# Performance work log

Hardware: AMD Instinct MI355X
Metric: run time of the kernel (lower is better)

Reference implementation:

```python
import jax, jax.numpy as jnp
import numpy as np

INT_MIN = jnp.iinfo(jnp.int32).min


def setup_inputs() -> dict:
    key = jax.random.key(0)
    ks = jax.random.split(key, 12)
    N, E, H, R, T = 200000, 100000, 100, 172, 100
    return {
        'src': jax.random.randint(ks[0], (E,), 0, N, dtype=jnp.int32),
        'dst': jax.random.randint(ks[1], (E,), 0, N, dtype=jnp.int32),
        't': jax.random.randint(ks[2], (E,), 0, 1000000, dtype=jnp.int32),
        'raw_msg': jax.random.normal(ks[3], (E, R), dtype=jnp.float32),
        'memory': jax.random.normal(ks[4], (N, H), dtype=jnp.float32),
        'last_update': jax.random.randint(ks[5], (N,), 0, 1000, dtype=jnp.int32),
        'te_w': jax.random.normal(ks[6], (T, 1), dtype=jnp.float32) * 0.1,
        'te_b': jax.random.normal(ks[7], (T,), dtype=jnp.float32) * 0.1,
        'w_ih': jax.random.normal(ks[8], (3 * H, 2 * H + R + T), dtype=jnp.float32) * 0.05,
        'w_hh': jax.random.normal(ks[9], (3 * H, H), dtype=jnp.float32) * 0.05,
        'b_ih': jax.random.normal(ks[10], (3 * H,), dtype=jnp.float32) * 0.05,
        'b_hh': jax.random.normal(ks[11], (3 * H,), dtype=jnp.float32) * 0.05,
    }


def reference(src, dst, t, raw_msg, memory, last_update, te_w, te_b, w_ih, w_hh, b_ih, b_hh):
    N, H = memory.shape
    E = src.shape[0]

    def time_enc(t_rel):  # Linear(1, time_dim) then cos, t_rel: [E] float
        return jnp.cos(t_rel[:, None] * te_w[:, 0][None, :] + te_b[None, :])

    # IdentityMessage: concat(mem[src], mem[dst], raw_msg, t_enc); two streams (s and d)
    t_enc_s = time_enc((t - last_update[src]).astype(raw_msg.dtype))
    t_enc_d = time_enc((t - last_update[dst]).astype(raw_msg.dtype))
    msg_s = jnp.concatenate([memory[src], memory[dst], raw_msg, t_enc_s], axis=-1)
    msg_d = jnp.concatenate([memory[dst], memory[src], raw_msg, t_enc_d], axis=-1)

    msg = jnp.concatenate([msg_s, msg_d], axis=0)        # [2E, msg_dim]
    idx = jnp.concatenate([src, dst], axis=0)            # [2E]
    t2 = jnp.concatenate([t, t], axis=0)                 # [2E]

    # LastAggregator: per node pick the message with maximum timestamp
    max_t = jnp.full((N,), INT_MIN, dtype=t2.dtype).at[idx].max(t2)
    cand = jnp.where(t2 == max_t[idx], jnp.arange(2 * E, dtype=jnp.int32), jnp.int32(-1))
    win = jnp.full((N,), -1, dtype=jnp.int32).at[idx].max(cand)  # winning edge per node
    has_msg = win >= 0
    aggr = jnp.where(has_msg[:, None], msg[jnp.clip(win, 0)], 0.0)  # [N, msg_dim]

    # GRUCell(msg_dim, H)
    gi = aggr @ w_ih.T + b_ih                             # [N, 3H]
    gh = memory @ w_hh.T + b_hh                           # [N, 3H]
    i_r, i_z, i_n = jnp.split(gi, 3, axis=-1)
    h_r, h_z, h_n = jnp.split(gh, 3, axis=-1)
    r = jax.nn.sigmoid(i_r + h_r)
    z = jax.nn.sigmoid(i_z + h_z)
    n = jnp.tanh(i_n + r * h_n)
    memory_new = (1.0 - z) * n + z * memory               # [N, H]

    last_update_new = last_update.at[idx].max(t2)         # scatter latest event time
    return memory_new, last_update_new
```

## Files before the change

kernel.cpp:

```cpp
#include <hip/hip_runtime.h>
#include <math.h>

typedef __attribute__((ext_vector_type(8))) short  short8;
typedef __attribute__((ext_vector_type(4))) float  f32x4;

static constexpr int H     = 100;
static constexpr int RD    = 172;
static constexpr int WK    = 472;
static constexpr int MSTR  = 104;
static constexpr int RSTR  = 176;
static constexpr int NKS   = 20;
static constexpr int MB    = 32;
static constexpr int GRPS  = 2;
static constexpr int BLK   = 448;
static constexpr int NTT   = 28;
static constexpr int BPK_N = NTT * NKS * 64 * 8;

static constexpr int FB_MB = 48;
static constexpr int FB_GR = 3;

__device__ inline unsigned short f2bf(float x) {
    union { float f; unsigned u; } v; v.f = x;
    return (unsigned short)((v.u + 0x7FFFu + ((v.u >> 16) & 1u)) >> 16);
}
__device__ inline float bf2f(unsigned short b) {
    union { unsigned u; float f; } v; v.u = ((unsigned)b) << 16;
    return v.f;
}
__device__ inline unsigned pkbf(float a, float b) {
    unsigned r;
    asm("v_cvt_pk_bf16_f32 %0, %1, %2" : "=v"(r) : "v"(a), "v"(b));
    return r;
}
__device__ inline float frcp(float x) {
    float r;
    asm("v_rcp_f32 %0, %1" : "=v"(r) : "v"(x));
    return r;
}
__device__ inline f32x4 mfma16(short8 a, short8 b, f32x4 c) {
    return __builtin_amdgcn_mfma_f32_16x16x32_bf16(a, b, c, 0, 0, 0);
}
__device__ inline float4 ld4g(const float* base, int lc, int limit) {
    if (lc + 4 <= limit) return *(const float4*)(base + lc);
    return make_float4(0.f, 0.f, 0.f, 0.f);
}
__device__ inline void gl16(const unsigned short* g, unsigned short* l) {
    __builtin_amdgcn_global_load_lds(
        (const __attribute__((address_space(1))) void*)g,
        (__attribute__((address_space(3))) void*)l, 16, 0, 0);
}

__global__ __launch_bounds__(256) void k_init(int* __restrict__ maxt, int* __restrict__ win,
                                              int* __restrict__ zb, int N) {
    int i = blockIdx.x * blockDim.x + threadIdx.x;
    if (i < N) { maxt[i] = (int)0x80000000; win[i] = -1; }
    if (i < 128) zb[i] = 0;
}
__global__ __launch_bounds__(256) void k_maxt(const int* __restrict__ src, const int* __restrict__ dst,
                                              const int* __restrict__ t, int* __restrict__ maxt, int E) {
    int j = blockIdx.x * blockDim.x + threadIdx.x;
    if (j < E) {
        int tj = t[j];
        atomicMax(&maxt[src[j]], tj);
        atomicMax(&maxt[dst[j]], tj);
    }
}
__global__ __launch_bounds__(256) void k_win(const int* __restrict__ src, const int* __restrict__ dst,
                                             const int* __restrict__ t, const int* __restrict__ maxt,
                                             int* __restrict__ win, int E) {
    int j = blockIdx.x * blockDim.x + threadIdx.x;
    if (j < E) {
        int tj = t[j];
        int s = src[j], d = dst[j];
        if (maxt[s] == tj) atomicMax(&win[s], j);
        if (maxt[d] == tj) atomicMax(&win[d], j + E);
    }
}
__global__ __launch_bounds__(256) void k_meta(const int* __restrict__ src, const int* __restrict__ dst,
                                              const int* __restrict__ t, const int* __restrict__ last_update,
                                              const int* __restrict__ win, int4* __restrict__ meta,
                                              float* __restrict__ out_lu, int E, int N) {
    int i = blockIdx.x * blockDim.x + threadIdx.x;
    if (i >= N) return;
    int lu = last_update[i], w = win[i];
    int j = 0, other = 0, has = 0, te = lu; float dt = 0.f;
    if (w >= 0) {
        has = 1;
        int e = (w < E) ? w : (w - E);
        j = e;
        other = (w < E) ? dst[e] : src[e];
        te = t[e];
        dt = (float)(te - lu);
    }
    out_lu[i] = (float)(te > lu ? te : lu);
    int4 m; m.x = j; m.y = other; m.z = has; m.w = __float_as_int(dt);
    meta[i] = m;
}

__global__ __launch_bounds__(256) void k_cvt(const float* __restrict__ mem, const float* __restrict__ raw,
                                             unsigned short* __restrict__ memB, unsigned short* __restrict__ rawB,
                                             int N, int E) {
    int i = blockIdx.x * 256 + threadIdx.x;
    const int nm = N * 13;
    if (i < nm) {
        int row = i / 13, o = (i - row * 13) * 8;
        float4 a = ld4g(mem + (size_t)row * 100, o, 100);
        float4 b = ld4g(mem + (size_t)row * 100, o + 4, 100);
        int4 s; s.x = (int)pkbf(a.x, a.y); s.y = (int)pkbf(a.z, a.w);
        s.z = (int)pkbf(b.x, b.y); s.w = (int)pkbf(b.z, b.w);
        *(int4*)&memB[(size_t)row * MSTR + o] = s;
    } else if (i < nm + E * 22) {
        int k = i - nm;
        int row = k / 22, o = (k - row * 22) * 8;
        float4 a = ld4g(raw + (size_t)row * 172, o, 172);
        float4 b = ld4g(raw + (size_t)row * 172, o + 4, 172);
        int4 s; s.x = (int)pkbf(a.x, a.y); s.y = (int)pkbf(a.z, a.w);
        s.z = (int)pkbf(b.x, b.y); s.w = (int)pkbf(b.z, b.w);
        *(int4*)&rawB[(size_t)row * RSTR + o] = s;
    }
}

__global__ __launch_bounds__(256) void k_prep(const float* __restrict__ w_ih, const float* __restrict__ w_hh,
                                              unsigned short* __restrict__ B) {
    int idx = blockIdx.x * 256 + threadIdx.x;
    if (idx >= BPK_N) return;
    int jj   = idx & 7;
    int lane = (idx >> 3) & 63;
    int rest = idx >> 9;
    int ks   = rest % NKS;
    int tile = rest / NKS;
    int kk   = ks * 32 + ((lane >> 4) << 3) + jj;
    float v = 0.f;
    if (tile < 21) {
        int gate = tile / 7;
        int tcol = (tile % 7) * 16 + (lane & 15);
        if (tcol < 100) {
            if (kk < 512) {
                int col = -1;
                if (kk < 100)                   col = kk;
                else if (kk >= 104 && kk < 204) col = kk - 4;
                else if (kk >= 208 && kk < 380) col = kk - 8;
                else if (kk >= 384 && kk < 484) col = kk - 12;
                if (col >= 0) v = w_ih[(gate * 100 + tcol) * WK + col];
            } else {
                int khh = kk - 512;
                if (gate < 2 && khh < 100)
                    v = w_hh[(gate * 100 + tcol) * H + khh];
            }
        }
    } else {
        int tcol = (tile - 21) * 16 + (lane & 15);
        int khh  = kk - 512;
        if (tcol < 100 && khh >= 0 && khh < 100)
            v = w_hh[(200 + tcol) * H + khh];
    }
    B[idx] = f2bf(v);
}

__global__ __launch_bounds__(BLK, 7) void k_gru2(
    const unsigned short* __restrict__ memB, const unsigned short* __restrict__ rawB,
    const float* __restrict__ te_w, const float* __restrict__ te_b,
    const float* __restrict__ b_ih, const float* __restrict__ b_hh,
    const int4* __restrict__ meta, const unsigned short* __restrict__ zb,
    const unsigned short* __restrict__ Bpack,
    float* __restrict__ out_mem, int N)
{
    __shared__ unsigned short sA[GRPS * NKS * 512];

    const int tid  = threadIdx.x;
    const int wv   = tid >> 6;
    const int lane = tid & 63;
    const int q    = lane >> 4;
    const int row  = lane & 15;
    const int node0 = blockIdx.x * MB;

#pragma unroll
    for (int g = 0; g < GRPS; ++g) {
        const int node_g = node0 + g * 16 + row;
        const bool val = node_g < N;
        const int4 m = val ? meta[node_g] : make_int4(0, 0, 0, 0);
        const bool has = m.z != 0;
        const float dt = __int_as_float(m.w);
        const unsigned short* pmm = has ? memB + (size_t)node_g * MSTR : zb;
        const unsigned short* pot = has ? memB + (size_t)m.y * MSTR   : zb;
        const unsigned short* prw = has ? rawB + (size_t)m.x * RSTR   : zb;
        const unsigned short* phh = val ? memB + (size_t)node_g * MSTR : zb;

#pragma unroll
        for (int ii = 0; ii < 3; ++ii) {
            const int ks = wv + 7 * ii;
            if (ks < NKS && (ks < 12 || ks >= 16)) {
                const int k0 = ks * 32 + q * 8;
                const unsigned short* s =
                    (k0 < 104) ? pmm + k0 :
                    (k0 < 208) ? pot + (k0 - 104) :
                    (k0 < 384) ? prw + (k0 - 208) :
                                 phh + (k0 - 512);
                gl16(s, &sA[(g * NKS + ks) * 512]);
            }
        }
#pragma unroll
        for (int ii = 0; ii < 3; ++ii) {
            const int ks = wv + 7 * ii;
            if (ks >= 12 && ks < 16) {
                const int o = (ks - 12) * 32 + q * 8;
                float4 w0 = ld4g(te_w, o, 100), w1 = ld4g(te_w, o + 4, 100);
                float4 c0 = ld4g(te_b, o, 100), c1 = ld4g(te_b, o + 4, 100);
                const float hf = has ? 1.f : 0.f;
                float v0 = hf * __cosf(fmaf(dt, w0.x, c0.x));
                float v1 = hf * __cosf(fmaf(dt, w0.y, c0.y));
                float v2 = hf * __cosf(fmaf(dt, w0.z, c0.z));
                float v3 = hf * __cosf(fmaf(dt, w0.w, c0.w));
                float v4 = hf * __cosf(fmaf(dt, w1.x, c1.x));
                float v5 = hf * __cosf(fmaf(dt, w1.y, c1.y));
                float v6 = hf * __cosf(fmaf(dt, w1.z, c1.z));
                float v7 = hf * __cosf(fmaf(dt, w1.w, c1.w));
                int4 sv;
                sv.x = (int)pkbf(v0, v1); sv.y = (int)pkbf(v2, v3);
                sv.z = (int)pkbf(v4, v5); sv.w = (int)pkbf(v6, v7);
                *(int4*)&sA[(g * NKS + ks) * 512 + lane * 8] = sv;
            }
        }
    }
    __syncthreads();

    f32x4 ar[GRPS], az[GRPS], an[GRPS], ah[GRPS];
#pragma unroll
    for (int m = 0; m < GRPS; ++m) { ar[m] = (f32x4)0.f; az[m] = (f32x4)0.f; an[m] = (f32x4)0.f; ah[m] = (f32x4)0.f; }

    __builtin_amdgcn_s_setprio(1);
#pragma unroll
    for (int ks = 0; ks < NKS; ++ks) {
        short8 a0 = *(const short8*)&sA[(0 * NKS + ks) * 512 + lane * 8];
        short8 a1 = *(const short8*)&sA[(1 * NKS + ks) * 512 + lane * 8];
        short8 br = *(const short8*)&Bpack[(((size_t)(     wv) * NKS + ks) * 64 + lane) * 8];
        short8 bz = *(const short8*)&Bpack[(((size_t)( 7 + wv) * NKS + ks) * 64 + lane) * 8];
        short8 bn = (ks < 16)
                  ? *(const short8*)&Bpack[(((size_t)(14 + wv) * NKS + ks) * 64 + lane) * 8]
                  : *(const short8*)&Bpack[(((size_t)(21 + wv) * NKS + ks) * 64 + lane) * 8];
        ar[0] = mfma16(a0, br, ar[0]);  ar[1] = mfma16(a1, br, ar[1]);
        az[0] = mfma16(a0, bz, az[0]);  az[1] = mfma16(a1, bz, az[1]);
        if (ks < 16) { an[0] = mfma16(a0, bn, an[0]);  an[1] = mfma16(a1, bn, an[1]); }
        else         { ah[0] = mfma16(a0, bn, ah[0]);  ah[1] = mfma16(a1, bn, ah[1]); }
    }
    __builtin_amdgcn_s_setprio(0);

    const int c = wv * 16 + row;
    if (c < 100) {
        const float br_ = b_ih[c]       + b_hh[c];
        const float bz_ = b_ih[c + 100] + b_hh[c + 100];
        const float bin = b_ih[c + 200];
        const float bhn = b_hh[c + 200];
        const int ksh = 16 + (c >> 5);
        const int qh  = (c >> 3) & 3;
        const int e   = c & 7;
#pragma unroll
        for (int m = 0; m < GRPS; ++m) {
#pragma unroll
            for (int r = 0; r < 4; ++r) {
                const int node = node0 + m * 16 + q * 4 + r;
                if (node < N) {
                    const int rw = q * 4 + r;
                    const float h  = bf2f(sA[(m * NKS + ksh) * 512 + (qh * 16 + rw) * 8 + e]);
                    const float rg = frcp(1.f + __expf(-(ar[m][r] + br_)));
                    const float zg = frcp(1.f + __expf(-(az[m][r] + bz_)));
                    const float xn = an[m][r] + bin + rg * (ah[m][r] + bhn);
                    const float th = copysignf(1.f - 2.f * frcp(__expf(2.f * fabsf(xn)) + 1.f), xn);
                    out_mem[(size_t)node * H + c] = (1.f - zg) * th + zg * h;
                }
            }
        }
    }
}

__global__ __launch_bounds__(BLK, 4) void k_gru_fused(
    const int* __restrict__ src, const int* __restrict__ dst, const int* __restrict__ t,
    const float* __restrict__ raw_msg, const float* __restrict__ memory,
    const int* __restrict__ last_update, const float* __restrict__ te_w,
    const float* __restrict__ te_b, const float* __restrict__ b_ih,
    const float* __restrict__ b_hh, const int* __restrict__ win,
    const unsigned short* __restrict__ Bpack,
    float* __restrict__ out_mem, float* __restrict__ out_lu, int E, int N)
{
    __shared__ unsigned short sA[FB_GR * NKS * 512];
    __shared__ int   s_other[FB_MB];
    __shared__ int   s_j[FB_MB];
    __shared__ int   s_has[FB_MB];
    __shared__ float s_dt[FB_MB];

    const int tid   = threadIdx.x;
    const int node0 = blockIdx.x * FB_MB;

    if (tid < FB_MB) {
        int node = node0 + tid;
        int has = 0, j = 0, other = 0; float dt = 0.f;
        if (node < N) {
            int lu = last_update[node];
            int w  = win[node];
            int te = lu;
            if (w >= 0) {
                has = 1;
                int e = (w < E) ? w : (w - E);
                j = e;
                other = (w < E) ? dst[e] : src[e];
                te = t[e];
                dt = (float)(te - lu);
            }
            out_lu[node] = (float)(te > lu ? te : lu);
        }
        s_j[tid] = j; s_other[tid] = other; s_has[tid] = has; s_dt[tid] = dt;
    }
    __syncthreads();

    if (tid < 432) {
        const int nl    = tid % 48;
        const int c0    = tid / 48;
        const int node  = node0 + nl;
        const bool valid = node < N;
        const int has   = s_has[nl];
        const float* memN = memory + (size_t)node * H;
        const float* memO = memory + (size_t)s_other[nl] * H;
        const float* rawJ = raw_msg + (size_t)s_j[nl] * RD;
        const float dt  = s_dt[nl];
        const int grp = nl >> 4;
        const int row = nl & 15;

        float4 va[8], vb[8];
#pragma unroll
        for (int it = 0; it < 8; ++it) {
            const int cc = c0 + it * 9;
            va[it] = make_float4(0.f, 0.f, 0.f, 0.f); vb[it] = va[it];
            if (cc < 67) {
                const int c = cc + 13, kb = c * 8;
                if (c < 26)      { if (has)  { va[it] = ld4g(memO, kb - 104, 100); vb[it] = ld4g(memO, kb - 100, 100); } }
                else if (c < 48) { if (has)  { va[it] = ld4g(rawJ, kb - 208, RD ); vb[it] = ld4g(rawJ, kb - 204, RD ); } }
                else if (c < 64) { }
                else             { if (valid){ va[it] = ld4g(memN, kb - 512, 100); vb[it] = ld4g(memN, kb - 508, 100); } }
            }
        }
#pragma unroll
        for (int it = 0; it < 8; ++it) {
            const int cc = c0 + it * 9;
            if (cc < 67) {
                const int c = cc + 13;
                if (c >= 48 && c < 64 && has) {
                    const int lc = c * 8 - 384;
                    float vv[8];
#pragma unroll
                    for (int x = 0; x < 8; ++x) {
                        int col = lc + x;
                        vv[x] = (col < 100) ? __cosf(fmaf(dt, te_w[col], te_b[col])) : 0.f;
                    }
                    va[it] = make_float4(vv[0], vv[1], vv[2], vv[3]);
                    vb[it] = make_float4(vv[4], vv[5], vv[6], vv[7]);
                }
                int4 sv;
                sv.x = (int)pkbf(va[it].x, va[it].y);
                sv.y = (int)pkbf(va[it].z, va[it].w);
                sv.z = (int)pkbf(vb[it].x, vb[it].y);
                sv.w = (int)pkbf(vb[it].z, vb[it].w);
                {
                    const int ks = c >> 2, sub = c & 3;
                    *(int4*)&sA[((grp * NKS + ks) * 64 + sub * 16 + row) * 8] = sv;
                }
                if (c >= 64 && c < 77) {
                    int4 sm_;
                    sm_.x = has ? sv.x : 0; sm_.y = has ? sv.y : 0;
                    sm_.z = has ? sv.z : 0; sm_.w = has ? sv.w : 0;
                    const int cm = c - 64;
                    const int ks = cm >> 2, sub = cm & 3;
                    *(int4*)&sA[((grp * NKS + ks) * 64 + sub * 16 + row) * 8] = sm_;
                }
            }
        }
    }
    __syncthreads();

    const int wv   = tid >> 6;
    const int lane = tid & 63;
    const int lrow = lane & 15;
    const int lhi  = lane >> 4;

    f32x4 ar[FB_GR], az[FB_GR], an[FB_GR], ah[FB_GR];
#pragma unroll
    for (int m = 0; m < FB_GR; ++m) { ar[m] = (f32x4)0.f; az[m] = (f32x4)0.f; an[m] = (f32x4)0.f; ah[m] = (f32x4)0.f; }

    __builtin_amdgcn_s_setprio(1);
#pragma unroll
    for (int ks = 0; ks < NKS; ++ks) {
        short8 a0 = *(const short8*)&sA[(0 * NKS + ks) * 512 + lane * 8];
        short8 a1 = *(const short8*)&sA[(1 * NKS + ks) * 512 + lane * 8];
        short8 a2 = *(const short8*)&sA[(2 * NKS + ks) * 512 + lane * 8];
        short8 br = *(const short8*)&Bpack[(((size_t)(     wv) * NKS + ks) * 64 + lane) * 8];
        short8 bz = *(const short8*)&Bpack[(((size_t)( 7 + wv) * NKS + ks) * 64 + lane) * 8];
        short8 bn = (ks < 16)
                  ? *(const short8*)&Bpack[(((size_t)(14 + wv) * NKS + ks) * 64 + lane) * 8]
                  : *(const short8*)&Bpack[(((size_t)(21 + wv) * NKS + ks) * 64 + lane) * 8];
        ar[0] = mfma16(a0, br, ar[0]);  ar[1] = mfma16(a1, br, ar[1]);  ar[2] = mfma16(a2, br, ar[2]);
        az[0] = mfma16(a0, bz, az[0]);  az[1] = mfma16(a1, bz, az[1]);  az[2] = mfma16(a2, bz, az[2]);
        if (ks < 16) { an[0] = mfma16(a0, bn, an[0]);  an[1] = mfma16(a1, bn, an[1]);  an[2] = mfma16(a2, bn, an[2]); }
        else         { ah[0] = mfma16(a0, bn, ah[0]);  ah[1] = mfma16(a1, bn, ah[1]);  ah[2] = mfma16(a2, bn, ah[2]); }
    }
    __builtin_amdgcn_s_setprio(0);

    const int c = wv * 16 + lrow;
    if (c < 100) {
        const float br_ = b_ih[c]       + b_hh[c];
        const float bz_ = b_ih[c + 100] + b_hh[c + 100];
        const float bin = b_ih[c + 200];
        const float bhn = b_hh[c + 200];
        const int ksh = 16 + (c >> 5);
        const int qh  = (c >> 3) & 3;
        const int e   = c & 7;
#pragma unroll
        for (int m = 0; m < FB_GR; ++m) {
#pragma unroll
            for (int r = 0; r < 4; ++r) {
                const int node = node0 + m * 16 + lhi * 4 + r;
                if (node < N) {
                    const int rw = lhi * 4 + r;
                    const float h  = bf2f(sA[(m * NKS + ksh) * 512 + (qh * 16 + rw) * 8 + e]);
                    const float rg = frcp(1.f + __expf(-(ar[m][r] + br_)));
                    const float zg = frcp(1.f + __expf(-(az[m][r] + bz_)));
                    const float xn = an[m][r] + bin + rg * (ah[m][r] + bhn);
                    const float th = copysignf(1.f - 2.f * frcp(__expf(2.f * fabsf(xn)) + 1.f), xn);
                    out_mem[(size_t)node * H + c] = (1.f - zg) * th + zg * h;
                }
            }
        }
    }
}

extern "C" void kernel_launch(void* const* d_in, const int* in_sizes, int n_in,
                              void* d_out, int out_size, void* d_ws, size_t ws_size,
                              hipStream_t stream)
{
    const int*   src         = (const int*)d_in[0];
    const int*   dst         = (const int*)d_in[1];
    const int*   t           = (const int*)d_in[2];
    const float* raw_msg     = (const float*)d_in[3];
    const float* memory      = (const float*)d_in[4];
    const int*   last_update = (const int*)d_in[5];
    const float* te_w        = (const float*)d_in[6];
    const float* te_b        = (const float*)d_in[7];
    const float* w_ih        = (const float*)d_in[8];
    const float* w_hh        = (const float*)d_in[9];
    const float* b_ih        = (const float*)d_in[10];
    const float* b_hh        = (const float*)d_in[11];

    const int E = in_sizes[0];
    const int N = in_sizes[5];

    float* out    = (float*)d_out;
    float* out_lu = out + (size_t)N * H;

    char* ws = (char*)d_ws;
    int* maxt = (int*)ws;
    int* win  = maxt + N;
    unsigned short* Bpack = (unsigned short*)(win + N);
    int4* meta = (int4*)(Bpack + BPK_N);
    unsigned short* zb   = (unsigned short*)(meta + N);
    unsigned short* memB = zb + 256;
    unsigned short* rawB = memB + (size_t)N * MSTR + 32;
    const size_t need = (size_t)((char*)(rawB + (size_t)E * RSTR) - ws) + 64;

    k_init<<<(N + 255) / 256, 256, 0, stream>>>(maxt, win, (int*)zb, N);
    k_prep<<<(BPK_N + 255) / 256, 256, 0, stream>>>(w_ih, w_hh, Bpack);
    k_maxt<<<(E + 255) / 256, 256, 0, stream>>>(src, dst, t, maxt, E);
    k_win <<<(E + 255) / 256, 256, 0, stream>>>(src, dst, t, maxt, win, E);

    if (ws_size >= need) {
        const int ncvt = N * 13 + E * 22;
        k_cvt<<<(ncvt + 255) / 256, 256, 0, stream>>>(memory, raw_msg, memB, rawB, N, E);
        k_meta<<<(N + 255) / 256, 256, 0, stream>>>(src, dst, t, last_update, win, meta, out_lu, E, N);
        k_gru2<<<(N + MB - 1) / MB, BLK, 0, stream>>>(memB, rawB, te_w, te_b, b_ih, b_hh,
                                                      meta, zb, Bpack, out, N);
    } else {
        k_gru_fused<<<(N + FB_MB - 1) / FB_MB, BLK, 0, stream>>>(src, dst, t, raw_msg, memory, last_update,
                                                                 te_w, te_b, b_ih, b_hh, win, Bpack,
                                                                 out, out_lu, E, N);
    }
}
```

Baseline: 205.8 us.

## Merge init/prep/convert kernels and software-pipeline B-tile loads in GRU MFMA loop

Merges k_init, k_prep and k_cvt into one k_pre launch, which removes two kernel launches and their serialization gaps. Inside k_gru2 the per-k-step global loads of the weight fragments are now double-buffered: the next step's B fragments are fetched before the current step's MFMAs, with a sched_barrier to stop the compiler reordering them. The launch-bounds occupancy hint drops from 7 to 4 waves to allow more registers for the prefetch buffers. The cost is lower occupancy and more register pressure.

```diff
diff --git a/kernel.cpp b/kernel.cpp
--- a/kernel.cpp
+++ b/kernel.cpp
@@ -50,12 +50,78 @@
         (__attribute__((address_space(3))) void*)l, 16, 0, 0);
 }
 
-__global__ __launch_bounds__(256) void k_init(int* __restrict__ maxt, int* __restrict__ win,
-                                              int* __restrict__ zb, int N) {
-    int i = blockIdx.x * blockDim.x + threadIdx.x;
+__global__ __launch_bounds__(256) void k_pre(
+    const float* __restrict__ mem, const float* __restrict__ raw,
+    const float* __restrict__ w_ih, const float* __restrict__ w_hh,
+    unsigned short* __restrict__ memB, unsigned short* __restrict__ rawB,
+    unsigned short* __restrict__ B, int* __restrict__ maxt, int* __restrict__ win,
+    int* __restrict__ zb, int N, int E, int docvt)
+{
+    int i = blockIdx.x * 256 + threadIdx.x;
+    if (docvt) {
+        const int nm = N * 13;
+        if (i < nm) {
+            int row = i / 13, o = (i - row * 13) * 8;
+            float4 a = ld4g(mem + (size_t)row * 100, o, 100);
+            float4 b = ld4g(mem + (size_t)row * 100, o + 4, 100);
+            int4 s; s.x = (int)pkbf(a.x, a.y); s.y = (int)pkbf(a.z, a.w);
+            s.z = (int)pkbf(b.x, b.y); s.w = (int)pkbf(b.z, b.w);
+            *(int4*)&memB[(size_t)row * MSTR + o] = s;
+            return;
+        }
+        i -= nm;
+        const int nr = E * 22;
+        if (i < nr) {
+            int row = i / 22, o = (i - row * 22) * 8;
+            float4 a = ld4g(raw + (size_t)row * 172, o, 172);
+            float4 b = ld4g(raw + (size_t)row * 172, o + 4, 172);
+            int4 s; s.x = (int)pkbf(a.x, a.y); s.y = (int)pkbf(a.z, a.w);
+            s.z = (int)pkbf(b.x, b.y); s.w = (int)pkbf(b.z, b.w);
+            *(int4*)&rawB[(size_t)row * RSTR + o] = s;
+            return;
+        }
+        i -= nr;
+    }
+    if (i < BPK_N) {
+        int idx  = i;
+        int jj   = idx & 7;
+        int lane = (idx >> 3) & 63;
+        int rest = idx >> 9;
+        int ks   = rest % NKS;
+        int tile = rest / NKS;
+        int kk   = ks * 32 + ((lane >> 4) << 3) + jj;
+        float v = 0.f;
+        if (tile < 21) {
+            int gate = tile / 7;
+            int tcol = (tile % 7) * 16 + (lane & 15);
+            if (tcol < 100) {
+                if (kk < 512) {
+                    int col = -1;
+                    if (kk < 100)                   col = kk;
+                    else if (kk >= 104 && kk < 204) col = kk - 4;
+                    else if (kk >= 208 && kk < 380) col = kk - 8;
+                    else if (kk >= 384 && kk < 484) col = kk - 12;
+                    if (col >= 0) v = w_ih[(gate * 100 + tcol) * WK + col];
+                } else {
+                    int khh = kk - 512;
+                    if (gate < 2 && khh < 100)
+                        v = w_hh[(gate * 100 + tcol) * H + khh];
+                }
+            }
+        } else {
+            int tcol = (tile - 21) * 16 + (lane & 15);
+            int khh  = kk - 512;
+            if (tcol < 100 && khh >= 0 && khh < 100)
+                v = w_hh[(200 + tcol) * H + khh];
+        }
+        B[idx] = f2bf(v);
+        return;
+    }
+    i -= BPK_N;
     if (i < N) { maxt[i] = (int)0x80000000; win[i] = -1; }
     if (i < 128) zb[i] = 0;
 }
+
 __global__ __launch_bounds__(256) void k_maxt(const int* __restrict__ src, const int* __restrict__ dst,
                                               const int* __restrict__ t, int* __restrict__ maxt, int E) {
     int j = blockIdx.x * blockDim.x + threadIdx.x;
@@ -97,67 +163,9 @@
     meta[i] = m;
 }
 
-__global__ __launch_bounds__(256) void k_cvt(const float* __restrict__ mem, const float* __restrict__ raw,
-                                             unsigned short* __restrict__ memB, unsigned short* __restrict__ rawB,
-                                             int N, int E) {
-    int i = blockIdx.x * 256 + threadIdx.x;
-    const int nm = N * 13;
-    if (i < nm) {
-        int row = i / 13, o = (i - row * 13) * 8;
-        float4 a = ld4g(mem + (size_t)row * 100, o, 100);
-        float4 b = ld4g(mem + (size_t)row * 100, o + 4, 100);
-        int4 s; s.x = (int)pkbf(a.x, a.y); s.y = (int)pkbf(a.z, a.w);
-        s.z = (int)pkbf(b.x, b.y); s.w = (int)pkbf(b.z, b.w);
-        *(int4*)&memB[(size_t)row * MSTR + o] = s;
-    } else if (i < nm + E * 22) {
-        int k = i - nm;
-        int row = k / 22, o = (k - row * 22) * 8;
-        float4 a = ld4g(raw + (size_t)row * 172, o, 172);
-        float4 b = ld4g(raw + (size_t)row * 172, o + 4, 172);
-        int4 s; s.x = (int)pkbf(a.x, a.y); s.y = (int)pkbf(a.z, a.w);
-        s.z = (int)pkbf(b.x, b.y); s.w = (int)pkbf(b.z, b.w);
-        *(int4*)&rawB[(size_t)row * RSTR + o] = s;
-    }
-}
-
-__global__ __launch_bounds__(256) void k_prep(const float* __restrict__ w_ih, const float* __restrict__ w_hh,
-                                              unsigned short* __restrict__ B) {
-    int idx = blockIdx.x * 256 + threadIdx.x;
-    if (idx >= BPK_N) return;
-    int jj   = idx & 7;
-    int lane = (idx >> 3) & 63;
-    int rest = idx >> 9;
-    int ks   = rest % NKS;
-    int tile = rest / NKS;
-    int kk   = ks * 32 + ((lane >> 4) << 3) + jj;
-    float v = 0.f;
-    if (tile < 21) {
-        int gate = tile / 7;
-        int tcol = (tile % 7) * 16 + (lane & 15);
-        if (tcol < 100) {
-            if (kk < 512) {
-                int col = -1;
-                if (kk < 100)                   col = kk;
-                else if (kk >= 104 && kk < 204) col = kk - 4;
-                else if (kk >= 208 && kk < 380) col = kk - 8;
-                else if (kk >= 384 && kk < 484) col = kk - 12;
-                if (col >= 0) v = w_ih[(gate * 100 + tcol) * WK + col];
-            } else {
-                int khh = kk - 512;
-                if (gate < 2 && khh < 100)
-                    v = w_hh[(gate * 100 + tcol) * H + khh];
-            }
-        }
-    } else {
-        int tcol = (tile - 21) * 16 + (lane & 15);
-        int khh  = kk - 512;
-        if (tcol < 100 && khh >= 0 && khh < 100)
-            v = w_hh[(200 + tcol) * H + khh];
-    }
-    B[idx] = f2bf(v);
-}
-
-__global__ __launch_bounds__(BLK, 7) void k_gru2(
+#define LB(tile, ks) (*(const short8*)&Bpack[(((size_t)(tile) * NKS + (ks)) * 64 + lane) * 8])
+
+__global__ __launch_bounds__(BLK, 4) void k_gru2(
     const unsigned short* __restrict__ memB, const unsigned short* __restrict__ rawB,
     const float* __restrict__ te_w, const float* __restrict__ te_b,
     const float* __restrict__ b_ih, const float* __restrict__ b_hh,
@@ -228,20 +236,27 @@
 #pragma unroll
     for (int m = 0; m < GRPS; ++m) { ar[m] = (f32x4)0.f; az[m] = (f32x4)0.f; an[m] = (f32x4)0.f; ah[m] = (f32x4)0.f; }
 
+    short8 cr = LB(wv, 0);
+    short8 cz = LB(7 + wv, 0);
+    short8 cn = LB(14 + wv, 0);
+
     __builtin_amdgcn_s_setprio(1);
 #pragma unroll
     for (int ks = 0; ks < NKS; ++ks) {
+        short8 nr = cr, nz = cz, nn2 = cn;
+        if (ks + 1 < NKS) {
+            nr  = LB(wv, ks + 1);
+            nz  = LB(7 + wv, ks + 1);
+            nn2 = LB((ks + 1 < 16) ? (14 + wv) : (21 + wv), ks + 1);
+        }
         short8 a0 = *(const short8*)&sA[(0 * NKS + ks) * 512 + lane * 8];
         short8 a1 = *(const short8*)&sA[(1 * NKS + ks) * 512 + lane * 8];
-        short8 br = *(const short8*)&Bpack[(((size_t)(     wv) * NKS + ks) * 64 + lane) * 8];
-        short8 bz = *(const short8*)&Bpack[(((size_t)( 7 + wv) * NKS + ks) * 64 + lane) * 8];
-        short8 bn = (ks < 16)
-                  ? *(const short8*)&Bpack[(((size_t)(14 + wv) * NKS + ks) * 64 + lane) * 8]
-                  : *(const short8*)&Bpack[(((size_t)(21 + wv) * NKS + ks) * 64 + lane) * 8];
-        ar[0] = mfma16(a0, br, ar[0]);  ar[1] = mfma16(a1, br, ar[1]);
-        az[0] = mfma16(a0, bz, az[0]);  az[1] = mfma16(a1, bz, az[1]);
-        if (ks < 16) { an[0] = mfma16(a0, bn, an[0]);  an[1] = mfma16(a1, bn, an[1]); }
-        else         { ah[0] = mfma16(a0, bn, ah[0]);  ah[1] = mfma16(a1, bn, ah[1]); }
+        __builtin_amdgcn_sched_barrier(0);
+        ar[0] = mfma16(a0, cr, ar[0]);  ar[1] = mfma16(a1, cr, ar[1]);
+        az[0] = mfma16(a0, cz, az[0]);  az[1] = mfma16(a1, cz, az[1]);
+        if (ks < 16) { an[0] = mfma16(a0, cn, an[0]);  an[1] = mfma16(a1, cn, an[1]); }
+        else         { ah[0] = mfma16(a0, cn, ah[0]);  ah[1] = mfma16(a1, cn, ah[1]); }
+        cr = nr; cz = nz; cn = nn2;
     }
     __builtin_amdgcn_s_setprio(0);
 
@@ -391,11 +406,9 @@
         short8 a0 = *(const short8*)&sA[(0 * NKS + ks) * 512 + lane * 8];
         short8 a1 = *(const short8*)&sA[(1 * NKS + ks) * 512 + lane * 8];
         short8 a2 = *(const short8*)&sA[(2 * NKS + ks) * 512 + lane * 8];
-        short8 br = *(const short8*)&Bpack[(((size_t)(     wv) * NKS + ks) * 64 + lane) * 8];
-        short8 bz = *(const short8*)&Bpack[(((size_t)( 7 + wv) * NKS + ks) * 64 + lane) * 8];
-        short8 bn = (ks < 16)
-                  ? *(const short8*)&Bpack[(((size_t)(14 + wv) * NKS + ks) * 64 + lane) * 8]
-                  : *(const short8*)&Bpack[(((size_t)(21 + wv) * NKS + ks) * 64 + lane) * 8];
+        short8 br = LB(wv, ks);
+        short8 bz = LB(7 + wv, ks);
+        short8 bn = (ks < 16) ? LB(14 + wv, ks) : LB(21 + wv, ks);
         ar[0] = mfma16(a0, br, ar[0]);  ar[1] = mfma16(a1, br, ar[1]);  ar[2] = mfma16(a2, br, ar[2]);
         az[0] = mfma16(a0, bz, az[0]);  az[1] = mfma16(a1, bz, az[1]);  az[2] = mfma16(a2, bz, az[2]);
         if (ks < 16) { an[0] = mfma16(a0, bn, an[0]);  an[1] = mfma16(a1, bn, an[1]);  an[2] = mfma16(a2, bn, an[2]); }
@@ -464,18 +477,21 @@
     unsigned short* rawB = memB + (size_t)N * MSTR + 32;
     const size_t need = (size_t)((char*)(rawB + (size_t)E * RSTR) - ws) + 64;
 
-    k_init<<<(N + 255) / 256, 256, 0, stream>>>(maxt, win, (int*)zb, N);
-    k_prep<<<(BPK_N + 255) / 256, 256, 0, stream>>>(w_ih, w_hh, Bpack);
-    k_maxt<<<(E + 255) / 256, 256, 0, stream>>>(src, dst, t, maxt, E);
-    k_win <<<(E + 255) / 256, 256, 0, stream>>>(src, dst, t, maxt, win, E);
-
     if (ws_size >= need) {
-        const int ncvt = N * 13 + E * 22;
-        k_cvt<<<(ncvt + 255) / 256, 256, 0, stream>>>(memory, raw_msg, memB, rawB, N, E);
+        const int npre = N * 13 + E * 22 + BPK_N + N;
+        k_pre <<<(npre + 255) / 256, 256, 0, stream>>>(memory, raw_msg, w_ih, w_hh,
+                                                       memB, rawB, Bpack, maxt, win, (int*)zb, N, E, 1);
+        k_maxt<<<(E + 255) / 256, 256, 0, stream>>>(src, dst, t, maxt, E);
+        k_win <<<(E + 255) / 256, 256, 0, stream>>>(src, dst, t, maxt, win, E);
         k_meta<<<(N + 255) / 256, 256, 0, stream>>>(src, dst, t, last_update, win, meta, out_lu, E, N);
         k_gru2<<<(N + MB - 1) / MB, BLK, 0, stream>>>(memB, rawB, te_w, te_b, b_ih, b_hh,
                                                       meta, zb, Bpack, out, N);
     } else {
+        const int npre = BPK_N + N;
+        k_pre <<<(npre + 255) / 256, 256, 0, stream>>>(memory, raw_msg, w_ih, w_hh,
+                                                       Bpack, Bpack, Bpack, maxt, win, (int*)zb, N, E, 0);
+        k_maxt<<<(E + 255) / 256, 256, 0, stream>>>(src, dst, t, maxt, E);
+        k_win <<<(E + 255) / 256, 256, 0, stream>>>(src, dst, t, maxt, win, E);
         k_gru_fused<<<(N + FB_MB - 1) / FB_MB, BLK, 0, stream>>>(src, dst, t, raw_msg, memory, last_update,
                                                                  te_w, te_b, b_ih, b_hh, win, Bpack,
                                                                  out, out_lu, E, N);
```

New measurement: 196.6 us. 4.5% less time.
